# Kernel tuning notes

Measured on AMD Instinct MI355X. Metric: run time of the kernel, lower is better.

Reference implementation:

```python
import math
import jax, jax.numpy as jnp
from jax import lax
import numpy as np

B, HH, WW = 8, 128, 128
N = HH * WW
DIM, NH = 256, 4
HD = DIM // 2 // NH          # 32, per-head dim of the halved channels
CH = DIM // 2                # 128
THETA, MAXSEQ = 10000.0, 4096

# --- static FoPE frequency setup (mirrors RotaryEmbedding.get_inv_freq with fope=True) ---
def _inv_freq():
    rot = 2 * HD                                   # rotary dim = d_model//n_heads = 2*head_dim
    inv = 1.0 / THETA ** (np.arange(0, rot, 2, dtype=np.float64) / rot)
    return inv[inv >= 2.0 * np.pi / MAXSEQ].astype(np.float32)

INV_FREQ = _inv_freq()
D_IN = int(INV_FREQ.shape[0])                      # 23
D_OUT = D_IN if D_IN <= (2 * HD) // 4 else (2 * HD) // 4   # 16


def _coef(key, gain=0.5):
    # xavier_normal_ on (NH, D_IN, D_OUT) + step-eye offset, as in FourierEmbedding.__init__
    fan_in, fan_out = D_IN * D_OUT, NH * D_OUT
    std = gain * math.sqrt(2.0 / (fan_in + fan_out))
    c = std * jax.random.normal(key, (NH, D_IN, D_OUT), jnp.float32)
    step = math.ceil(D_IN / D_OUT)
    eye = np.zeros((NH, D_IN, D_OUT), np.float32)
    for i in range(D_OUT):
        if i * step < D_IN:
            eye[:, i * step, i] = 1.0
    return c + jnp.asarray(eye)


def setup_inputs() -> dict:
    key = jax.random.key(0)
    ks = jax.random.split(key, 10)
    def lin(k, o, i):
        lim = 1.0 / math.sqrt(i)
        return jax.random.uniform(k, (o, i), jnp.float32, -lim, lim)
    return {
        "x": jax.random.normal(ks[0], (B, N, DIM), jnp.float32),
        "Wq": lin(ks[1], CH, DIM), "bq": jnp.zeros((CH,), jnp.float32),
        "Wk": lin(ks[2], CH, DIM), "bk": jnp.zeros((CH,), jnp.float32),
        "Wv": lin(ks[3], CH, DIM), "bv": jnp.zeros((CH,), jnp.float32),
        # Hedgehog maps init as identity
        "Whq": jnp.eye(HD, dtype=jnp.float32), "bhq": jnp.zeros((HD,), jnp.float32),
        "Whk": jnp.eye(HD, dtype=jnp.float32), "bhk": jnp.zeros((HD,), jnp.float32),
        "sin_coef": _coef(ks[4]), "cos_coef": _coef(ks[5]),
        "lepe_w": 0.02 * jax.random.normal(ks[6], (CH, 1, 3, 3), jnp.float32),
        "lepe_b": jnp.zeros((CH,), jnp.float32),
        "temperature": jnp.ones((CH, 1), jnp.float32),
        "Wp": lin(ks[7], DIM, DIM), "bp": jnp.zeros((DIM,), jnp.float32),
        "h": HH, "w": WW,
    }


def _hedgehog(t, W, b):
    # t: [b,h,n,HD] -> [b,h,n,2*HD]
    y = jnp.einsum('bhnd,ed->bhne', t, W) + b
    return jax.nn.softmax(jnp.concatenate([2.0 * y, -2.0 * y], axis=-1), axis=-1)


def _fope(t, sin_coef, cos_coef, n):
    # t: [b,h,n,2*HD]; learnable Fourier rotary
    freqs = jnp.arange(n, dtype=jnp.float32)[:, None] * jnp.asarray(INV_FREQ)[None, :]  # [n,D_IN]
    cs = sin_coef / sin_coef.sum(axis=-2, keepdims=True)
    cc = cos_coef / cos_coef.sum(axis=-2, keepdims=True)
    fs = jnp.einsum('tD,hDd->htd', jnp.sin(freqs), cs)[None]   # [1,h,n,D_OUT]
    fc = jnp.einsum('tD,hDd->htd', jnp.cos(freqs), cc)[None]
    pad = ((0, 0), (0, 0), (0, 0), (0, HD - D_OUT))
    fs = jnp.pad(fs, pad, constant_values=1.0)
    fc = jnp.pad(fc, pad, constant_values=1.0)
    fs = jnp.concatenate([fs, fs], axis=-1)                    # [1,h,n,2*HD]
    fc = jnp.concatenate([fc, fc], axis=-1)
    x1, x2 = t[..., :HD], t[..., HD:]
    rot = jnp.concatenate([-x2, x1], axis=-1)
    return t * fc - rot * fs


def _forward(x, Wq, bq, Wk, bk, Wv, bv, Whq, bhq, Whk, bhk,
             sin_coef, cos_coef, lepe_w, lepe_b, temperature, Wp, bp, h, w):
    b, n, _ = x.shape
    q = x @ Wq.T + bq   # [b,n,CH]
    k = x @ Wk.T + bk
    v = x @ Wv.T + bv

    # ---- spatial brand (Hedgehog linear attention with Fourier rotary) ----
    qh = q.reshape(b, n, NH, HD).swapaxes(1, 2)   # [b,nh,n,HD]
    kh = k.reshape(b, n, NH, HD).swapaxes(1, 2)
    vh = v.reshape(b, n, NH, HD).swapaxes(1, 2)
    qf = _hedgehog(qh, Whq, bhq)                  # [b,nh,n,2HD]
    kf = _hedgehog(kh, Whk, bhk)
    q_fope = _fope(qf, sin_coef, cos_coef, n)
    k_fope = _fope(kf, sin_coef, cos_coef, n)
    kmean = kf.mean(axis=-2, keepdims=True)                       # [b,nh,1,2HD]
    z = 1.0 / (jnp.einsum('bhnd,bhsd->bhns', qf, kmean) + 1e-6)   # [b,nh,n,1]
    s = n ** (-0.5)
    kv = jnp.einsum('bhnd,bhne->bhde', k_fope * s, vh * s)        # [b,nh,2HD,HD]
    xs = jnp.einsum('bhnd,bhde->bhne', q_fope, kv) * z            # [b,nh,n,HD]
    xs = xs.swapaxes(1, 2).reshape(b, n, CH)
    v_img = vh.swapaxes(-1, -2).reshape(b, CH, h, w)
    conv = lax.conv_general_dilated(v_img, lepe_w, (1, 1), 'SAME',
                                    feature_group_count=CH,
                                    dimension_numbers=('NCHW', 'OIHW', 'NCHW'))
    conv = conv + lepe_b[None, :, None, None]
    x_spatial = conv.reshape(b, CH, n).transpose(0, 2, 1) + xs    # [b,n,CH]

    # ---- channel brand (transposed attention over channels) ----
    qc = q.swapaxes(-1, -2)   # [b,CH,n]
    kc = k.swapaxes(-1, -2)
    vc = v.swapaxes(-1, -2)
    qn = qc / jnp.maximum(jnp.linalg.norm(qc, axis=-1, keepdims=True), 1e-12)
    kn = kc / jnp.maximum(jnp.linalg.norm(kc, axis=-1, keepdims=True), 1e-12)
    attn = jax.nn.softmax(jnp.einsum('bcl,bdl->bcd', qn, kn) * temperature, axis=-1)
    x_channel = jnp.einsum('bcd,bdl->bcl', attn, vc).swapaxes(-1, -2)  # [b,n,CH]

    out = jnp.concatenate([x_spatial, x_channel], axis=-1) @ Wp.T + bp  # [b,n,DIM]
    return out, q, k


def reference(x, Wq, bq, Wk, bk, Wv, bv, Whq, bhq, Whk, bhk,
              sin_coef, cos_coef, lepe_w, lepe_b, temperature, Wp, bp, h, w):
    return _forward(x, Wq, bq, Wk, bk, Wv, bv, Whq, bhq, Whk, bhk,
                    sin_coef, cos_coef, lepe_w, lepe_b, temperature, Wp, bp, h, w)
```

## Files before the change

kernel.cpp:

```cpp
#include <hip/hip_runtime.h>
#include <cmath>

#define NB 8
#define NN 16384
#define DIN 23
#define DOUT 16

typedef short bf16x8 __attribute__((ext_vector_type(8)));
typedef float f32x4 __attribute__((ext_vector_type(4)));

__device__ __forceinline__ unsigned short f2bf(float f) {
    unsigned int u = __float_as_uint(f);
    u += 0x7FFFu + ((u >> 16) & 1u);
    return (unsigned short)(u >> 16);
}
__device__ __forceinline__ float bf2f(unsigned short s) {
    return __uint_as_float(((unsigned int)s) << 16);
}
__device__ __forceinline__ float rcpf(float x) { return __builtin_amdgcn_rcpf(x); }

__device__ __forceinline__ bf16x8 cvt8(float4 a, float4 b) {
    bf16x8 r;
    r[0]=(short)f2bf(a.x); r[1]=(short)f2bf(a.y); r[2]=(short)f2bf(a.z); r[3]=(short)f2bf(a.w);
    r[4]=(short)f2bf(b.x); r[5]=(short)f2bf(b.y); r[6]=(short)f2bf(b.z); r[7]=(short)f2bf(b.w);
    return r;
}
__device__ __forceinline__ void red16(f32x4& s) {
    #pragma unroll
    for (int off = 1; off < 16; off <<= 1) {
        s[0] += __shfl_xor(s[0], off); s[1] += __shfl_xor(s[1], off);
        s[2] += __shfl_xor(s[2], off); s[3] += __shfl_xor(s[3], off);
    }
}
__device__ __forceinline__ void red16x2(f32x4& s, f32x4& w) {
    #pragma unroll
    for (int off = 1; off < 16; off <<= 1) {
        s[0] += __shfl_xor(s[0], off); s[1] += __shfl_xor(s[1], off);
        s[2] += __shfl_xor(s[2], off); s[3] += __shfl_xor(s[3], off);
        w[0] += __shfl_xor(w[0], off); w[1] += __shfl_xor(w[1], off);
        w[2] += __shfl_xor(w[2], off); w[3] += __shfl_xor(w[3], off);
    }
}

#define WS_XSP    ((size_t)0)
#define WS_VB     ((size_t)16777216)
#define WS_XSB    ((size_t)25165824)
#define WS_FS     ((size_t)33554432)
#define WS_INV    ((size_t)35651584)
#define WS_CS     ((size_t)35651648)
#define WS_CC     ((size_t)35653184)
#define WS_WCAT   ((size_t)35654720)
#define WS_BCAT   ((size_t)35703872)
#define WS_KVPART ((size_t)35704256)
#define WS_KMPART ((size_t)37801408)
#define WS_KV     ((size_t)37866944)
#define WS_KMEAN  ((size_t)37932480)
#define WS_QN2    ((size_t)37934528)
#define WS_KN2    ((size_t)37935552)
#define WS_G      ((size_t)37936576)
#define WS_ATTN   ((size_t)38067648)
#define WS_BMATT  ((size_t)38198720)
#define WS_QB     ((size_t)38460864)
#define WS_KB     ((size_t)46849472)

__global__ void k_setup(const float* __restrict__ sc, const float* __restrict__ ccin,
                        float* __restrict__ inv, float* __restrict__ cs, float* __restrict__ cc)
{
    int t = threadIdx.x;
    if (t < DIN) inv[t] = (float)pow(10000.0, -((double)(2 * t)) / 64.0);
    int h = t >> 4, d = t & 15;
    float ss = 0.f, s2 = 0.f;
    for (int D = 0; D < DIN; ++D) { ss += sc[(h*DIN + D)*DOUT + d]; s2 += ccin[(h*DIN + D)*DOUT + d]; }
    float rs = 1.f / ss, r2 = 1.f / s2;
    for (int D = 0; D < DIN; ++D) {
        cs[(h*DIN + D)*DOUT + d] = sc[(h*DIN + D)*DOUT + d] * rs;
        cc[(h*DIN + D)*DOUT + d] = ccin[(h*DIN + D)*DOUT + d] * r2;
    }
}

__global__ __launch_bounds__(256) void k_tables(const float* __restrict__ inv, const float* __restrict__ cs,
                                                const float* __restrict__ cc,
                                                unsigned int* __restrict__ fsc)
{
    int t = threadIdx.x;
    int sub = t >> 6, lane = t & 63;
    int tpos = blockIdx.x*4 + sub;
    __shared__ float ssin[4][DIN], scos[4][DIN];
    if (lane < DIN) { float fr = (float)tpos * inv[lane]; ssin[sub][lane] = sinf(fr); scos[sub][lane] = cosf(fr); }
    __syncthreads();
    int h = lane >> 4, d = lane & 15;
    float as = 0.f, ac = 0.f;
    for (int D = 0; D < DIN; ++D) { as += ssin[sub][D]*cs[(h*DIN + D)*DOUT + d]; ac += scos[sub][D]*cc[(h*DIN + D)*DOUT + d]; }
    fsc[((size_t)h*NN + tpos)*16 + d] = ((unsigned int)f2bf(ac) << 16) | (unsigned int)f2bf(as);
}

__global__ __launch_bounds__(256) void k_wprep(
    const float* __restrict__ Wq, const float* __restrict__ Wk, const float* __restrict__ Wv,
    const float* __restrict__ bq, const float* __restrict__ bk, const float* __restrict__ bv,
    unsigned short* __restrict__ Wc, float* __restrict__ bcat)
{
    int row = blockIdx.x, t = threadIdx.x;
    const float* W = (row < 128) ? Wq : (row < 256) ? Wk : Wv;
    const float* bb = (row < 128) ? bq : (row < 256) ? bk : bv;
    int r = row & 127;
    Wc[(size_t)row*256 + t] = f2bf(W[(size_t)r*256 + t]);
    if (t == 0) bcat[row] = bb[r];
}

__global__ __launch_bounds__(256) void k_qkv_mfma(const float* __restrict__ x,
    const unsigned short* __restrict__ Wc, const float* __restrict__ bcat,
    float* __restrict__ q, float* __restrict__ k,
    unsigned short* __restrict__ qb, unsigned short* __restrict__ kb,
    unsigned short* __restrict__ vb)
{
    __shared__ unsigned short Asm[128*64];
    __shared__ unsigned short Bsm[128*64];
    int t = threadIdx.x;
    int lin = blockIdx.y*3 + blockIdx.x;
    int logical = (lin & 7)*384 + (lin >> 3);
    int ntile = logical % 3;
    int mtile = logical / 3;
    int m0 = mtile * 128;
    int n0 = ntile * 128;
    int wave = t >> 6, lane = t & 63;
    int wm = wave >> 1, wn = wave & 1;
    int lrow = lane & 15, lk = lane >> 4;
    f32x4 acc[4][4];
    #pragma unroll
    for (int i = 0; i < 4; ++i)
        #pragma unroll
        for (int j = 0; j < 4; ++j) acc[i][j] = (f32x4){0.f,0.f,0.f,0.f};

    int am = t >> 4, ak4 = t & 15;
    size_t arow = (size_t)(m0 + am);
    float4 pa[8];
    #pragma unroll
    for (int p = 0; p < 8; ++p)
        pa[p] = *reinterpret_cast<const float4*>(&x[(arow + p*16)*256 + ak4*4]);

    #pragma unroll
    for (int kt = 0; kt < 4; ++kt) {
        int k0 = kt * 64;
        if (kt) __syncthreads();
        #pragma unroll
        for (int p = 0; p < 8; ++p) {
            int m = am + p*16;
            ushort4 b4;
            b4.x = f2bf(pa[p].x); b4.y = f2bf(pa[p].y); b4.z = f2bf(pa[p].z); b4.w = f2bf(pa[p].w);
            int byte = m*128 + ((ak4*8) ^ ((m & 7) << 4));
            *reinterpret_cast<ushort4*>(reinterpret_cast<char*>(Asm) + byte) = b4;
        }
        {
            int n = t >> 3, k8 = t & 7;
            #pragma unroll
            for (int p = 0; p < 4; ++p, n += 32) {
                uint4 u4 = *reinterpret_cast<const uint4*>(&Wc[(size_t)(n0 + n)*256 + k0 + k8*8]);
                int byte = n*128 + ((k8 ^ (n & 7)) << 4);
                *reinterpret_cast<uint4*>(reinterpret_cast<char*>(Bsm) + byte) = u4;
            }
        }
        if (kt < 3) {
            #pragma unroll
            for (int p = 0; p < 8; ++p)
                pa[p] = *reinterpret_cast<const float4*>(&x[(arow + p*16)*256 + (kt+1)*64 + ak4*4]);
        }
        __syncthreads();
        #pragma unroll
        for (int ks = 0; ks < 2; ++ks) {
            bf16x8 af[4], bfv[4];
            #pragma unroll
            for (int mi = 0; mi < 4; ++mi) {
                int m = wm*64 + mi*16 + lrow;
                int u = (ks*4 + lk) ^ (m & 7);
                af[mi] = *reinterpret_cast<const bf16x8*>(reinterpret_cast<const char*>(Asm) + m*128 + u*16);
            }
            #pragma unroll
            for (int ni = 0; ni < 4; ++ni) {
                int n = wn*64 + ni*16 + lrow;
                int u = (ks*4 + lk) ^ (n & 7);
                bfv[ni] = *reinterpret_cast<const bf16x8*>(reinterpret_cast<const char*>(Bsm) + n*128 + u*16);
            }
            #pragma unroll
            for (int mi = 0; mi < 4; ++mi)
                #pragma unroll
                for (int ni = 0; ni < 4; ++ni)
                    acc[mi][ni] = __builtin_amdgcn_mfma_f32_16x16x32_bf16(af[mi], bfv[ni], acc[mi][ni], 0, 0, 0);
        }
    }
    #pragma unroll
    for (int mi = 0; mi < 4; ++mi) {
        #pragma unroll
        for (int ni = 0; ni < 4; ++ni) {
            int gcol = n0 + wn*64 + ni*16 + lrow;
            int c = gcol & 127;
            float bias = bcat[gcol];
            #pragma unroll
            for (int r = 0; r < 4; ++r) {
                size_t grow = (size_t)m0 + wm*64 + mi*16 + lk*4 + r;
                float val = acc[mi][ni][r] + bias;
                if (ntile == 0)      { q[grow*128 + c] = val; qb[grow*128 + c] = f2bf(val); }
                else if (ntile == 1) { k[grow*128 + c] = val; kb[grow*128 + c] = f2bf(val); }
                else                 vb[grow*128 + c] = f2bf(val);
            }
        }
    }
}

__global__ __launch_bounds__(256) void k_conv(const unsigned short* __restrict__ vb, const float* __restrict__ w,
                                              const float* __restrict__ bias, float* __restrict__ xsp)
{
    __shared__ float wsmT[9][128];
    __shared__ float bsm[128];
    int t = threadIdx.x;
    for (int i = t; i < 1152; i += 256) wsmT[i % 9][i / 9] = w[i];
    if (t < 128) bsm[t] = bias[t];
    __syncthreads();
    int jj = t >> 4, c8 = (t & 15) * 8;
    int j = blockIdx.x * 16 + jj;
    int i = blockIdx.y, b = blockIdx.z;
    float acc[8];
    #pragma unroll
    for (int l = 0; l < 8; ++l) acc[l] = bsm[c8 + l];
    #pragma unroll
    for (int di = 0; di < 3; ++di) {
        int ii = i + di - 1;
        if (ii < 0 || ii >= 128) continue;
        #pragma unroll
        for (int dj = 0; dj < 3; ++dj) {
            int jx = j + dj - 1;
            if (jx < 0 || jx >= 128) continue;
            uint4 u = *reinterpret_cast<const uint4*>(&vb[((size_t)b*NN + ii*128 + jx)*128 + c8]);
            const unsigned short* us = (const unsigned short*)&u;
            int kk = di*3 + dj;
            #pragma unroll
            for (int l = 0; l < 8; ++l)
                acc[l] += wsmT[kk][c8 + l] * bf2f(us[l]);
        }
    }
    float4 r0 = {acc[0],acc[1],acc[2],acc[3]}, r1 = {acc[4],acc[5],acc[6],acc[7]};
    size_t ob = ((size_t)b*NN + i*128 + j)*128 + c8;
    *reinterpret_cast<float4*>(&xsp[ob]) = r0;
    *reinterpret_cast<float4*>(&xsp[ob+4]) = r1;
}

__global__ __launch_bounds__(256) void k_featkv(
    const unsigned short* __restrict__ kb, const unsigned short* __restrict__ vb,
    const float* __restrict__ W, const float* __restrict__ bvec,
    const unsigned int* __restrict__ fsc,
    float* __restrict__ kvpart, float* __restrict__ kmpart)
{
    __shared__ __align__(16) unsigned short kfsT[4][64][72];
    __shared__ __align__(16) unsigned short vT[4][32][72];
    __shared__ float kms[4][64];
    int bh = blockIdx.y, b = bh >> 2, h = bh & 3;
    int chunk = blockIdx.x;
    int t = threadIdx.x, w = t >> 6, lane = t & 63;
    int c = lane & 15, g = lane >> 4;
    bf16x8 wb[2];
    #pragma unroll
    for (int et = 0; et < 2; ++et) {
        float4 wa = *reinterpret_cast<const float4*>(&W[(c + et*16)*32 + g*8]);
        float4 wb2 = *reinterpret_cast<const float4*>(&W[(c + et*16)*32 + g*8 + 4]);
        wb[et] = cvt8(wa, wb2);
    }
    float bias0 = bvec[c], bias1 = bvec[c + 16];
    f32x4 acc[4][2];
    #pragma unroll
    for (int i = 0; i < 4; ++i) { acc[i][0] = (f32x4){0.f,0.f,0.f,0.f}; acc[i][1] = (f32x4){0.f,0.f,0.f,0.f}; }
    f32x4 km0 = {0.f,0.f,0.f,0.f}, km1 = km0, km2 = km0, km3 = km0;

    for (int rnd = 0; rnd < 2; ++rnd) {
        int p0 = chunk*512 + w*128 + rnd*64;
        {
            uint4 vr[4];
            size_t vbase = ((size_t)(b*NN + p0 + c*4))*128 + h*32 + g*8;
            #pragma unroll
            for (int i = 0; i < 4; ++i) vr[i] = *reinterpret_cast<const uint4*>(&vb[vbase + (size_t)i*128]);
            #pragma unroll
            for (int j = 0; j < 8; ++j) {
                ushort4 pk;
                pk.x = ((const unsigned short*)&vr[0])[j];
                pk.y = ((const unsigned short*)&vr[1])[j];
                pk.z = ((const unsigned short*)&vr[2])[j];
                pk.w = ((const unsigned short*)&vr[3])[j];
                *reinterpret_cast<ushort4*>(&vT[w][g*8 + j][c*4]) = pk;
            }
        }
        #pragma unroll
        for (int mt = 0; mt < 4; ++mt) {
            int posA = p0 + mt*16 + c;
            bf16x8 af = *reinterpret_cast<const bf16x8*>(&kb[((size_t)(b*NN + posA))*128 + h*32 + g*8]);
            f32x4 z4 = {0.f,0.f,0.f,0.f};
            f32x4 y0 = __builtin_amdgcn_mfma_f32_16x16x32_bf16(af, wb[0], z4, 0, 0, 0);
            f32x4 y1 = __builtin_amdgcn_mfma_f32_16x16x32_bf16(af, wb[1], z4, 0, 0, 0);
            f32x4 el0, eh0, el1, eh1;
            #pragma unroll
            for (int r = 0; r < 4; ++r) {
                float a0 = 2.f*(y0[r] + bias0);
                float a1 = 2.f*(y1[r] + bias1);
                el0[r] = __expf(a0); eh0[r] = __expf(-a0);
                el1[r] = __expf(a1); eh1[r] = __expf(-a1);
            }
            f32x4 s = el0 + eh0 + el1 + eh1;
            red16(s);
            f32x4 rs;
            #pragma unroll
            for (int r = 0; r < 4; ++r) rs[r] = rcpf(s[r]);
            f32x4 klo0 = el0*rs, khi0 = eh0*rs, klo1 = el1*rs, khi1 = eh1*rs;
            km0 += klo0; km1 += khi0; km2 += klo1; km3 += khi1;
            int posC = p0 + mt*16 + g*4;
            ushort4 wlo0, whi0, wlo1, whi1;
            #pragma unroll
            for (int r = 0; r < 4; ++r) {
                unsigned int u = fsc[((size_t)h*NN + posC + r)*16 + c];
                float fsv = bf2f((unsigned short)(u & 0xffffu));
                float fcv = bf2f((unsigned short)(u >> 16));
                ((unsigned short*)&wlo0)[r] = f2bf(klo0[r]*fcv + khi0[r]*fsv);
                ((unsigned short*)&whi0)[r] = f2bf(khi0[r]*fcv - klo0[r]*fsv);
                ((unsigned short*)&wlo1)[r] = f2bf(klo1[r] + khi1[r]);
                ((unsigned short*)&whi1)[r] = f2bf(khi1[r] - klo1[r]);
            }
            int po = mt*16 + g*4;
            *reinterpret_cast<ushort4*>(&kfsT[w][c][po])      = wlo0;
            *reinterpret_cast<ushort4*>(&kfsT[w][32 + c][po]) = whi0;
            *reinterpret_cast<ushort4*>(&kfsT[w][16 + c][po]) = wlo1;
            *reinterpret_cast<ushort4*>(&kfsT[w][48 + c][po]) = whi1;
        }
        #pragma unroll
        for (int ks = 0; ks < 2; ++ks) {
            bf16x8 bf0 = *reinterpret_cast<const bf16x8*>(&vT[w][c][ks*32 + g*8]);
            bf16x8 bf1 = *reinterpret_cast<const bf16x8*>(&vT[w][16 + c][ks*32 + g*8]);
            #pragma unroll
            for (int mt = 0; mt < 4; ++mt) {
                bf16x8 af2 = *reinterpret_cast<const bf16x8*>(&kfsT[w][mt*16 + c][ks*32 + g*8]);
                acc[mt][0] = __builtin_amdgcn_mfma_f32_16x16x32_bf16(af2, bf0, acc[mt][0], 0, 0, 0);
                acc[mt][1] = __builtin_amdgcn_mfma_f32_16x16x32_bf16(af2, bf1, acc[mt][1], 0, 0, 0);
            }
        }
    }
    float kv0 = km0[0]+km0[1]+km0[2]+km0[3];
    float kv1 = km1[0]+km1[1]+km1[2]+km1[3];
    float kv2 = km2[0]+km2[1]+km2[2]+km2[3];
    float kv3 = km3[0]+km3[1]+km3[2]+km3[3];
    kv0 += __shfl_xor(kv0, 16); kv0 += __shfl_xor(kv0, 32);
    kv1 += __shfl_xor(kv1, 16); kv1 += __shfl_xor(kv1, 32);
    kv2 += __shfl_xor(kv2, 16); kv2 += __shfl_xor(kv2, 32);
    kv3 += __shfl_xor(kv3, 16); kv3 += __shfl_xor(kv3, 32);
    if (g == 0) {
        kms[w][c] = kv0; kms[w][16 + c] = kv2; kms[w][32 + c] = kv1; kms[w][48 + c] = kv3;
    }
    float* kvred = reinterpret_cast<float*>(&kfsT[0][0][0]);
    #pragma unroll
    for (int mt = 0; mt < 4; ++mt)
        #pragma unroll
        for (int nt = 0; nt < 2; ++nt) {
            int d = nt*16 + c;
            *reinterpret_cast<f32x4*>(&kvred[(size_t)(w*32 + d)*72 + mt*16 + g*4]) = acc[mt][nt];
        }
    __syncthreads();
    #pragma unroll
    for (int i = 0; i < 8; ++i) {
        int idx = t*8 + i;
        int f = idx >> 5, d = idx & 31;
        float s2 = kvred[(0*32 + d)*72 + f] + kvred[(1*32 + d)*72 + f]
                 + kvred[(2*32 + d)*72 + f] + kvred[(3*32 + d)*72 + f];
        kvpart[((size_t)(bh*32 + chunk))*2048 + idx] = s2;
    }
    if (t < 64) {
        float s2 = kms[0][t] + kms[1][t] + kms[2][t] + kms[3][t];
        kmpart[(size_t)(bh*32 + chunk)*64 + t] = s2;
    }
}

__global__ __launch_bounds__(256) void k_kvred2(const float* __restrict__ kvpart, unsigned short* __restrict__ kvT)
{
    int bh = blockIdx.x >> 3, part = blockIdx.x & 7;
    int idx = part*256 + threadIdx.x;
    float s = 0.f;
    for (int cidx = 0; cidx < 32; ++cidx) s += kvpart[((size_t)(bh*32 + cidx))*2048 + idx];
    int f = idx >> 5, d = idx & 31;
    kvT[(size_t)bh*2048 + d*64 + f] = f2bf(s * (1.f/16384.f));
}

__global__ __launch_bounds__(64) void k_kmred(const float* __restrict__ kmpart, float* __restrict__ kmean)
{
    int bh = blockIdx.x, t = threadIdx.x;
    float s = 0.f;
    for (int cidx = 0; cidx < 32; ++cidx) s += kmpart[(size_t)(bh*32 + cidx)*64 + t];
    kmean[bh*64 + t] = s * (1.f/16384.f);
}

__global__ __launch_bounds__(256) void k_featxs(
    const unsigned short* __restrict__ qb, const float* __restrict__ W, const float* __restrict__ bvec,
    const unsigned int* __restrict__ fsc, const unsigned short* __restrict__ kvT,
    const float* __restrict__ kmean, const float* __restrict__ xsp, unsigned short* __restrict__ xsb)
{
    __shared__ __align__(16) unsigned short qfs[4][64][72];
    int bh = blockIdx.y, b = bh >> 2, h = bh & 3;
    int chunk = blockIdx.x;
    int t = threadIdx.x, w = t >> 6, lane = t & 63;
    int c = lane & 15, g = lane >> 4;
    bf16x8 wb[2];
    #pragma unroll
    for (int et = 0; et < 2; ++et) {
        float4 wa = *reinterpret_cast<const float4*>(&W[(c + et*16)*32 + g*8]);
        float4 wb2 = *reinterpret_cast<const float4*>(&W[(c + et*16)*32 + g*8 + 4]);
        wb[et] = cvt8(wa, wb2);
    }
    float bias0 = bvec[c], bias1 = bvec[c + 16];
    float kml0 = kmean[bh*64 + c],      kml1 = kmean[bh*64 + 16 + c];
    float kmh0 = kmean[bh*64 + 32 + c], kmh1 = kmean[bh*64 + 48 + c];
    bf16x8 bkv[2][2];
    #pragma unroll
    for (int nt = 0; nt < 2; ++nt)
        #pragma unroll
        for (int ks = 0; ks < 2; ++ks)
            bkv[nt][ks] = *reinterpret_cast<const bf16x8*>(&kvT[(size_t)bh*2048 + (nt*16 + c)*64 + ks*32 + g*8]);

    for (int rnd = 0; rnd < 2; ++rnd) {
        int p0 = chunk*512 + w*128 + rnd*64;
        #pragma unroll
        for (int mt = 0; mt < 4; ++mt) {
            int posA = p0 + mt*16 + c;
            bf16x8 af = *reinterpret_cast<const bf16x8*>(&qb[((size_t)(b*NN + posA))*128 + h*32 + g*8]);
            f32x4 z4 = {0.f,0.f,0.f,0.f};
            f32x4 y0 = __builtin_amdgcn_mfma_f32_16x16x32_bf16(af, wb[0], z4, 0, 0, 0);
            f32x4 y1 = __builtin_amdgcn_mfma_f32_16x16x32_bf16(af, wb[1], z4, 0, 0, 0);
            f32x4 el0, eh0, el1, eh1;
            #pragma unroll
            for (int r = 0; r < 4; ++r) {
                float a0 = 2.f*(y0[r] + bias0);
                float a1 = 2.f*(y1[r] + bias1);
                el0[r] = __expf(a0); eh0[r] = __expf(-a0);
                el1[r] = __expf(a1); eh1[r] = __expf(-a1);
            }
            f32x4 s = el0 + eh0 + el1 + eh1;
            f32x4 wv = el0*kml0 + eh0*kmh0 + el1*kml1 + eh1*kmh1;
            red16x2(s, wv);
            f32x4 zr;
            #pragma unroll
            for (int r = 0; r < 4; ++r) {
                float rs = rcpf(s[r]);
                float z = rcpf(wv[r]*rs + 1e-6f);
                zr[r] = z*rs;
            }
            int posC = mt*16 + g*4;
            #pragma unroll
            for (int r = 0; r < 4; ++r) {
                unsigned int u = fsc[((size_t)h*NN + p0 + posC + r)*16 + c];
                float fsv = bf2f((unsigned short)(u & 0xffffu));
                float fcv = bf2f((unsigned short)(u >> 16));
                qfs[w][posC + r][c]      = f2bf(zr[r]*(el0[r]*fcv + eh0[r]*fsv));
                qfs[w][posC + r][32 + c] = f2bf(zr[r]*(eh0[r]*fcv - el0[r]*fsv));
                qfs[w][posC + r][16 + c] = f2bf(zr[r]*(el1[r] + eh1[r]));
                qfs[w][posC + r][48 + c] = f2bf(zr[r]*(eh1[r] - el1[r]));
            }
        }
        f32x4 acc[4][2];
        #pragma unroll
        for (int i = 0; i < 4; ++i) { acc[i][0] = (f32x4){0.f,0.f,0.f,0.f}; acc[i][1] = (f32x4){0.f,0.f,0.f,0.f}; }
        #pragma unroll
        for (int ks = 0; ks < 2; ++ks)
            #pragma unroll
            for (int mt = 0; mt < 4; ++mt) {
                bf16x8 af2 = *reinterpret_cast<const bf16x8*>(&qfs[w][mt*16 + c][ks*32 + g*8]);
                acc[mt][0] = __builtin_amdgcn_mfma_f32_16x16x32_bf16(af2, bkv[0][ks], acc[mt][0], 0, 0, 0);
                acc[mt][1] = __builtin_amdgcn_mfma_f32_16x16x32_bf16(af2, bkv[1][ks], acc[mt][1], 0, 0, 0);
            }
        #pragma unroll
        for (int mt = 0; mt < 4; ++mt)
            #pragma unroll
            for (int nt = 0; nt < 2; ++nt) {
                int d = nt*16 + c;
                #pragma unroll
                for (int r = 0; r < 4; ++r) {
                    int pos = p0 + mt*16 + g*4 + r;
                    size_t off = ((size_t)(b*NN + pos))*128 + h*32 + d;
                    xsb[off] = f2bf(xsp[off] + acc[mt][nt][r]);
                }
            }
    }
}

__global__ __launch_bounds__(256) void k_gram(const unsigned short* __restrict__ qb, const unsigned short* __restrict__ kb,
                                              float* __restrict__ Gpart,
                                              float* __restrict__ qn2, float* __restrict__ kn2)
{
    __shared__ unsigned short qTs[128][40];
    __shared__ unsigned short kTs[128][40];
    int kc = blockIdx.x, bb = blockIdx.y;
    int t = threadIdx.x, lane = t & 63;
    int wave = t >> 6, wm = wave >> 1, wn = wave & 1;
    int c = t & 127, lh = t >> 7;
    float qa = 0.f, ka = 0.f;
    f32x4 acc[4][4];
    #pragma unroll
    for (int i = 0; i < 4; ++i)
        #pragma unroll
        for (int j = 0; j < 4; ++j) acc[i][j] = (f32x4){0.f,0.f,0.f,0.f};

    for (int kt = 0; kt < 8; ++kt) {
        __syncthreads();
        #pragma unroll
        for (int i = 0; i < 16; ++i) {
            int l = lh*16 + i;
            size_t pos = (size_t)bb*NN + kc*256 + kt*32 + l;
            unsigned short qu = qb[pos*128 + c];
            unsigned short ku = kb[pos*128 + c];
            float qv = bf2f(qu), kvv = bf2f(ku);
            qa += qv*qv; ka += kvv*kvv;
            qTs[c][l] = qu;
            kTs[c][l] = ku;
        }
        __syncthreads();
        bf16x8 af[4];
        #pragma unroll
        for (int mi = 0; mi < 4; ++mi)
            af[mi] = *reinterpret_cast<const bf16x8*>(&qTs[wm*64 + mi*16 + (lane & 15)][(lane >> 4)*8]);
        #pragma unroll
        for (int ni = 0; ni < 4; ++ni) {
            bf16x8 bfr = *reinterpret_cast<const bf16x8*>(&kTs[wn*64 + ni*16 + (lane & 15)][(lane >> 4)*8]);
            #pragma unroll
            for (int mi = 0; mi < 4; ++mi)
                acc[mi][ni] = __builtin_amdgcn_mfma_f32_16x16x32_bf16(af[mi], bfr, acc[mi][ni], 0, 0, 0);
        }
    }
    size_t gb = ((size_t)(bb*64 + kc))*16384;
    #pragma unroll
    for (int mi = 0; mi < 4; ++mi) {
        #pragma unroll
        for (int ni = 0; ni < 4; ++ni) {
            int d = wn*64 + ni*16 + (lane & 15);
            #pragma unroll
            for (int r = 0; r < 4; ++r) {
                int cc = wm*64 + mi*16 + (lane >> 4)*4 + r;
                Gpart[gb + (size_t)cc*128 + d] = acc[mi][ni][r];
            }
        }
    }
    atomicAdd(&qn2[bb*128 + c], qa);
    atomicAdd(&kn2[bb*128 + c], ka);
}

__global__ __launch_bounds__(256) void k_gramred(const float* __restrict__ Gpart, float* __restrict__ G)
{
    int bb = blockIdx.y;
    int idx = blockIdx.x*256 + threadIdx.x;
    float s = 0.f;
    for (int kc = 0; kc < 64; ++kc) s += Gpart[((size_t)(bb*64 + kc))*16384 + idx];
    G[(size_t)bb*16384 + idx] = s;
}

__global__ __launch_bounds__(128) void k_attnsm(const float* __restrict__ G, const float* __restrict__ qn2,
    const float* __restrict__ kn2, const float* __restrict__ temp, float* __restrict__ attn)
{
    __shared__ float red[128];
    int row = blockIdx.x;
    int b = row >> 7, c = row & 127;
    int t = threadIdx.x;
    float qn = fmaxf(sqrtf(qn2[b*128 + c]), 1e-12f);
    float kn = fmaxf(sqrtf(kn2[b*128 + t]), 1e-12f);
    float val = G[(size_t)row*128 + t] / (qn*kn) * temp[c];
    red[t] = val; __syncthreads();
    for (int s = 64; s > 0; s >>= 1) { if (t < s) red[t] = fmaxf(red[t], red[t+s]); __syncthreads(); }
    float mm = red[0]; __syncthreads();
    float ev = expf(val - mm);
    red[t] = ev; __syncthreads();
    for (int s = 64; s > 0; s >>= 1) { if (t < s) red[t] += red[t+s]; __syncthreads(); }
    attn[(size_t)row*128 + t] = ev / red[0];
}

__global__ __launch_bounds__(256) void k_bmat(const float* __restrict__ attn, const float* __restrict__ Wp,
                                              unsigned short* __restrict__ BmatT)
{
    int b = blockIdx.y, kk = blockIdx.x, o = threadIdx.x;
    float val;
    if (kk < 128) {
        val = Wp[(size_t)o*256 + kk];
    } else {
        int d = kk - 128;
        __shared__ float a[128];
        if (o < 128) a[o] = attn[((size_t)b*128 + o)*128 + d];
        __syncthreads();
        float acc = 0.f;
        for (int c = 0; c < 128; ++c) acc += a[c] * Wp[(size_t)o*256 + 128 + c];
        val = acc;
    }
    BmatT[((size_t)b*256 + o)*256 + kk] = f2bf(val);
}

__global__ __launch_bounds__(256) void k_out_mfma(const unsigned short* __restrict__ xsb,
    const unsigned short* __restrict__ vb, const unsigned short* __restrict__ BmatT,
    const float* __restrict__ bp, float* __restrict__ out)
{
    __shared__ unsigned short Asm[128*64];
    __shared__ unsigned short Bsm[128*64];
    int t = threadIdx.x;
    int lin = blockIdx.y*2 + blockIdx.x;
    int logical = (lin & 7)*256 + (lin >> 3);
    int ntile = logical & 1;
    int mtile = logical >> 1;
    int m0 = mtile * 128;
    int n0 = ntile * 128;
    int b = mtile >> 7;
    int wave = t >> 6, lane = t & 63;
    int wm = wave >> 1, wn = wave & 1;
    int lrow = lane & 15, lk = lane >> 4;
    f32x4 acc[4][4];
    #pragma unroll
    for (int i = 0; i < 4; ++i)
        #pragma unroll
        for (int j = 0; j < 4; ++j) acc[i][j] = (f32x4){0.f,0.f,0.f,0.f};

    int am = t >> 3, ak8 = t & 7;
    uint4 pa4[4];
    #pragma unroll
    for (int p = 0; p < 4; ++p)
        pa4[p] = *reinterpret_cast<const uint4*>(&xsb[(size_t)(m0 + am + p*32)*128 + ak8*8]);

    #pragma unroll
    for (int kt = 0; kt < 4; ++kt) {
        if (kt) __syncthreads();
        #pragma unroll
        for (int p = 0; p < 4; ++p) {
            int m = am + p*32;
            int byte = m*128 + ((ak8 ^ (m & 7)) << 4);
            *reinterpret_cast<uint4*>(reinterpret_cast<char*>(Asm) + byte) = pa4[p];
        }
        {
            int n = t >> 3, k8 = t & 7;
            #pragma unroll
            for (int p = 0; p < 4; ++p, n += 32) {
                uint4 u4 = *reinterpret_cast<const uint4*>(&BmatT[((size_t)b*256 + n0 + n)*256 + kt*64 + k8*8]);
                int byte = n*128 + ((k8 ^ (n & 7)) << 4);
                *reinterpret_cast<uint4*>(reinterpret_cast<char*>(Bsm) + byte) = u4;
            }
        }
        if (kt < 3) {
            const unsigned short* Asrc = ((kt+1) < 2) ? xsb : vb;
            int ka0 = ((kt+1) & 1) * 64;
            #pragma unroll
            for (int p = 0; p < 4; ++p)
                pa4[p] = *reinterpret_cast<const uint4*>(&Asrc[(size_t)(m0 + am + p*32)*128 + ka0 + ak8*8]);
        }
        __syncthreads();
        #pragma unroll
        for (int ks = 0; ks < 2; ++ks) {
            bf16x8 af[4], bfv[4];
            #pragma unroll
            for (int mi = 0; mi < 4; ++mi) {
                int m = wm*64 + mi*16 + lrow;
                int u = (ks*4 + lk) ^ (m & 7);
                af[mi] = *reinterpret_cast<const bf16x8*>(reinterpret_cast<const char*>(Asm) + m*128 + u*16);
            }
            #pragma unroll
            for (int ni = 0; ni < 4; ++ni) {
                int n = wn*64 + ni*16 + lrow;
                int u = (ks*4 + lk) ^ (n & 7);
                bfv[ni] = *reinterpret_cast<const bf16x8*>(reinterpret_cast<const char*>(Bsm) + n*128 + u*16);
            }
            #pragma unroll
            for (int mi = 0; mi < 4; ++mi)
                #pragma unroll
                for (int ni = 0; ni < 4; ++ni)
                    acc[mi][ni] = __builtin_amdgcn_mfma_f32_16x16x32_bf16(af[mi], bfv[ni], acc[mi][ni], 0, 0, 0);
        }
    }
    #pragma unroll
    for (int mi = 0; mi < 4; ++mi) {
        #pragma unroll
        for (int ni = 0; ni < 4; ++ni) {
            int gcol = n0 + wn*64 + ni*16 + lrow;
            float bias = bp[gcol];
            #pragma unroll
            for (int r = 0; r < 4; ++r) {
                size_t grow = (size_t)m0 + wm*64 + mi*16 + lk*4 + r;
                out[grow*256 + gcol] = acc[mi][ni][r] + bias;
            }
        }
    }
}

extern "C" void kernel_launch(void* const* d_in, const int* in_sizes, int n_in,
                              void* d_out, int out_size, void* d_ws, size_t ws_size,
                              hipStream_t stream)
{
    (void)in_sizes; (void)n_in; (void)out_size; (void)ws_size;
    const float* x    = (const float*)d_in[0];
    const float* Wq   = (const float*)d_in[1];
    const float* bq   = (const float*)d_in[2];
    const float* Wk   = (const float*)d_in[3];
    const float* bk   = (const float*)d_in[4];
    const float* Wv   = (const float*)d_in[5];
    const float* bv   = (const float*)d_in[6];
    const float* Whq  = (const float*)d_in[7];
    const float* bhq  = (const float*)d_in[8];
    const float* Whk  = (const float*)d_in[9];
    const float* bhk  = (const float*)d_in[10];
    const float* sinc = (const float*)d_in[11];
    const float* cosc = (const float*)d_in[12];
    const float* lw   = (const float*)d_in[13];
    const float* lb   = (const float*)d_in[14];
    const float* temp = (const float*)d_in[15];
    const float* Wp   = (const float*)d_in[16];
    const float* bp   = (const float*)d_in[17];

    float* out = (float*)d_out;
    float* q   = out + 33554432;
    float* k   = out + 50331648;
    float* ws  = (float*)d_ws;

    float* xsp    = ws + WS_XSP;
    float* Gpart  = ws + WS_XSP;
    unsigned short* vbuf = (unsigned short*)(ws + WS_VB);
    unsigned short* xsb  = (unsigned short*)(ws + WS_XSB);
    unsigned int* fsc = (unsigned int*)(ws + WS_FS);
    float* inv    = ws + WS_INV;
    float* cs     = ws + WS_CS;
    float* cc     = ws + WS_CC;
    unsigned short* Wc = (unsigned short*)(ws + WS_WCAT);
    float* bcat   = ws + WS_BCAT;
    float* kvpart = ws + WS_KVPART;
    float* kmpart = ws + WS_KMPART;
    unsigned short* kvT = (unsigned short*)(ws + WS_KV);
    float* kmean  = ws + WS_KMEAN;
    float* qn2    = ws + WS_QN2;
    float* kn2    = ws + WS_KN2;
    float* G      = ws + WS_G;
    float* attn   = ws + WS_ATTN;
    unsigned short* BmatT = (unsigned short*)(ws + WS_BMATT);
    unsigned short* qbuf  = (unsigned short*)(ws + WS_QB);
    unsigned short* kbuf  = (unsigned short*)(ws + WS_KB);

    hipMemsetAsync(qn2, 0, 2048*sizeof(float), stream);

    k_setup<<<1, 64, 0, stream>>>(sinc, cosc, inv, cs, cc);
    k_tables<<<4096, 256, 0, stream>>>(inv, cs, cc, fsc);
    k_wprep<<<384, 256, 0, stream>>>(Wq, Wk, Wv, bq, bk, bv, Wc, bcat);
    k_qkv_mfma<<<dim3(3, 1024), 256, 0, stream>>>(x, Wc, bcat, q, k, qbuf, kbuf, vbuf);
    k_conv<<<dim3(8, 128, 8), 256, 0, stream>>>(vbuf, lw, lb, xsp);
    k_featkv<<<dim3(32, 32), 256, 0, stream>>>(kbuf, vbuf, Whk, bhk, fsc, kvpart, kmpart);
    k_kvred2<<<256, 256, 0, stream>>>(kvpart, kvT);
    k_kmred<<<32, 64, 0, stream>>>(kmpart, kmean);
    k_featxs<<<dim3(32, 32), 256, 0, stream>>>(qbuf, Whq, bhq, fsc, kvT, kmean, xsp, xsb);
    k_gram<<<dim3(64, 8), 256, 0, stream>>>(qbuf, kbuf, Gpart, qn2, kn2);
    k_gramred<<<dim3(64, 8), 256, 0, stream>>>(Gpart, G);
    k_attnsm<<<1024, 128, 0, stream>>>(G, qn2, kn2, temp, attn);
    k_bmat<<<dim3(256, 8), 256, 0, stream>>>(attn, Wp, BmatT);
    k_out_mfma<<<dim3(2, 1024), 256, 0, stream>>>(xsb, vbuf, BmatT, bp, out);
}
```

Baseline: 440.2 us.

## Store conv output as bf16, shrink feature tiles, fold reduction kernels

The depthwise conv output is now stored in bf16 instead of fp32, halving its write and later read traffic in the feature kernel. The featkv and featxs kernels process 32-position rounds instead of 64, which shrinks the shared-memory tiles and may raise occupancy. The kmean reduction is folded into kvred2 and the Gram partial reduction into the softmax kernel, removing two launches and the intermediate G buffer. The bf16 storage of the conv output adds rounding error before the residual add.

New measurement: 384.8 us, median of 4. 1.14x faster.

```diff
diff --git a/kernel.cpp b/kernel.cpp
--- a/kernel.cpp
+++ b/kernel.cpp
@@ -42,7 +42,8 @@
     }
 }
 
-#define WS_XSP    ((size_t)0)
+#define WS_XSPB   ((size_t)0)
+#define WS_GPART  ((size_t)8388608)
 #define WS_VB     ((size_t)16777216)
 #define WS_XSB    ((size_t)25165824)
 #define WS_FS     ((size_t)33554432)
@@ -57,7 +58,6 @@
 #define WS_KMEAN  ((size_t)37932480)
 #define WS_QN2    ((size_t)37934528)
 #define WS_KN2    ((size_t)37935552)
-#define WS_G      ((size_t)37936576)
 #define WS_ATTN   ((size_t)38067648)
 #define WS_BMATT  ((size_t)38198720)
 #define WS_QB     ((size_t)38460864)
@@ -207,7 +207,7 @@
 }
 
 __global__ __launch_bounds__(256) void k_conv(const unsigned short* __restrict__ vb, const float* __restrict__ w,
-                                              const float* __restrict__ bias, float* __restrict__ xsp)
+                                              const float* __restrict__ bias, unsigned short* __restrict__ xspb)
 {
     __shared__ float wsmT[9][128];
     __shared__ float bsm[128];
@@ -237,10 +237,12 @@
                 acc[l] += wsmT[kk][c8 + l] * bf2f(us[l]);
         }
     }
-    float4 r0 = {acc[0],acc[1],acc[2],acc[3]}, r1 = {acc[4],acc[5],acc[6],acc[7]};
+    ushort4 r0, r1;
+    r0.x = f2bf(acc[0]); r0.y = f2bf(acc[1]); r0.z = f2bf(acc[2]); r0.w = f2bf(acc[3]);
+    r1.x = f2bf(acc[4]); r1.y = f2bf(acc[5]); r1.z = f2bf(acc[6]); r1.w = f2bf(acc[7]);
     size_t ob = ((size_t)b*NN + i*128 + j)*128 + c8;
-    *reinterpret_cast<float4*>(&xsp[ob]) = r0;
-    *reinterpret_cast<float4*>(&xsp[ob+4]) = r1;
+    *reinterpret_cast<ushort4*>(&xspb[ob]) = r0;
+    *reinterpret_cast<ushort4*>(&xspb[ob+4]) = r1;
 }
 
 __global__ __launch_bounds__(256) void k_featkv(
@@ -249,13 +251,14 @@
     const unsigned int* __restrict__ fsc,
     float* __restrict__ kvpart, float* __restrict__ kmpart)
 {
-    __shared__ __align__(16) unsigned short kfsT[4][64][72];
-    __shared__ __align__(16) unsigned short vT[4][32][72];
+    __shared__ __align__(16) char smem[34816];
     __shared__ float kms[4][64];
     int bh = blockIdx.y, b = bh >> 2, h = bh & 3;
     int chunk = blockIdx.x;
     int t = threadIdx.x, w = t >> 6, lane = t & 63;
     int c = lane & 15, g = lane >> 4;
+    unsigned short* kfsTw = reinterpret_cast<unsigned short*>(smem) + w*2560;
+    unsigned short* vTw   = reinterpret_cast<unsigned short*>(smem + 20480) + w*1280;
     bf16x8 wb[2];
     #pragma unroll
     for (int et = 0; et < 2; ++et) {
@@ -269,25 +272,23 @@
     for (int i = 0; i < 4; ++i) { acc[i][0] = (f32x4){0.f,0.f,0.f,0.f}; acc[i][1] = (f32x4){0.f,0.f,0.f,0.f}; }
     f32x4 km0 = {0.f,0.f,0.f,0.f}, km1 = km0, km2 = km0, km3 = km0;
 
-    for (int rnd = 0; rnd < 2; ++rnd) {
-        int p0 = chunk*512 + w*128 + rnd*64;
+    for (int rnd = 0; rnd < 4; ++rnd) {
+        int p0 = chunk*512 + w*128 + rnd*32;
         {
-            uint4 vr[4];
-            size_t vbase = ((size_t)(b*NN + p0 + c*4))*128 + h*32 + g*8;
-            #pragma unroll
-            for (int i = 0; i < 4; ++i) vr[i] = *reinterpret_cast<const uint4*>(&vb[vbase + (size_t)i*128]);
+            uint4 vr0, vr1;
+            size_t vbase = ((size_t)(b*NN + p0 + c*2))*128 + h*32 + g*8;
+            vr0 = *reinterpret_cast<const uint4*>(&vb[vbase]);
+            vr1 = *reinterpret_cast<const uint4*>(&vb[vbase + 128]);
             #pragma unroll
             for (int j = 0; j < 8; ++j) {
-                ushort4 pk;
-                pk.x = ((const unsigned short*)&vr[0])[j];
-                pk.y = ((const unsigned short*)&vr[1])[j];
-                pk.z = ((const unsigned short*)&vr[2])[j];
-                pk.w = ((const unsigned short*)&vr[3])[j];
-                *reinterpret_cast<ushort4*>(&vT[w][g*8 + j][c*4]) = pk;
-            }
-        }
-        #pragma unroll
-        for (int mt = 0; mt < 4; ++mt) {
+                ushort2 pk;
+                pk.x = ((const unsigned short*)&vr0)[j];
+                pk.y = ((const unsigned short*)&vr1)[j];
+                *reinterpret_cast<ushort2*>(&vTw[(g*8 + j)*40 + c*2]) = pk;
+            }
+        }
+        #pragma unroll
+        for (int mt = 0; mt < 2; ++mt) {
             int posA = p0 + mt*16 + c;
             bf16x8 af = *reinterpret_cast<const bf16x8*>(&kb[((size_t)(b*NN + posA))*128 + h*32 + g*8]);
             f32x4 z4 = {0.f,0.f,0.f,0.f};
@@ -321,18 +322,17 @@
                 ((unsigned short*)&whi1)[r] = f2bf(khi1[r] - klo1[r]);
             }
             int po = mt*16 + g*4;
-            *reinterpret_cast<ushort4*>(&kfsT[w][c][po])      = wlo0;
-            *reinterpret_cast<ushort4*>(&kfsT[w][32 + c][po]) = whi0;
-            *reinterpret_cast<ushort4*>(&kfsT[w][16 + c][po]) = wlo1;
-            *reinterpret_cast<ushort4*>(&kfsT[w][48 + c][po]) = whi1;
-        }
-        #pragma unroll
-        for (int ks = 0; ks < 2; ++ks) {
-            bf16x8 bf0 = *reinterpret_cast<const bf16x8*>(&vT[w][c][ks*32 + g*8]);
-            bf16x8 bf1 = *reinterpret_cast<const bf16x8*>(&vT[w][16 + c][ks*32 + g*8]);
+            *reinterpret_cast<ushort4*>(&kfsTw[(c)*40 + po])      = wlo0;
+            *reinterpret_cast<ushort4*>(&kfsTw[(32 + c)*40 + po]) = whi0;
+            *reinterpret_cast<ushort4*>(&kfsTw[(16 + c)*40 + po]) = wlo1;
+            *reinterpret_cast<ushort4*>(&kfsTw[(48 + c)*40 + po]) = whi1;
+        }
+        {
+            bf16x8 bf0 = *reinterpret_cast<const bf16x8*>(&vTw[(c)*40 + g*8]);
+            bf16x8 bf1 = *reinterpret_cast<const bf16x8*>(&vTw[(16 + c)*40 + g*8]);
             #pragma unroll
             for (int mt = 0; mt < 4; ++mt) {
-                bf16x8 af2 = *reinterpret_cast<const bf16x8*>(&kfsT[w][mt*16 + c][ks*32 + g*8]);
+                bf16x8 af2 = *reinterpret_cast<const bf16x8*>(&kfsTw[(mt*16 + c)*40 + g*8]);
                 acc[mt][0] = __builtin_amdgcn_mfma_f32_16x16x32_bf16(af2, bf0, acc[mt][0], 0, 0, 0);
                 acc[mt][1] = __builtin_amdgcn_mfma_f32_16x16x32_bf16(af2, bf1, acc[mt][1], 0, 0, 0);
             }
@@ -349,21 +349,22 @@
     if (g == 0) {
         kms[w][c] = kv0; kms[w][16 + c] = kv2; kms[w][32 + c] = kv1; kms[w][48 + c] = kv3;
     }
-    float* kvred = reinterpret_cast<float*>(&kfsT[0][0][0]);
+    __syncthreads();
+    float* kvred = reinterpret_cast<float*>(smem);
     #pragma unroll
     for (int mt = 0; mt < 4; ++mt)
         #pragma unroll
         for (int nt = 0; nt < 2; ++nt) {
             int d = nt*16 + c;
-            *reinterpret_cast<f32x4*>(&kvred[(size_t)(w*32 + d)*72 + mt*16 + g*4]) = acc[mt][nt];
+            *reinterpret_cast<f32x4*>(&kvred[(size_t)(w*32 + d)*68 + mt*16 + g*4]) = acc[mt][nt];
         }
     __syncthreads();
     #pragma unroll
     for (int i = 0; i < 8; ++i) {
         int idx = t*8 + i;
         int f = idx >> 5, d = idx & 31;
-        float s2 = kvred[(0*32 + d)*72 + f] + kvred[(1*32 + d)*72 + f]
-                 + kvred[(2*32 + d)*72 + f] + kvred[(3*32 + d)*72 + f];
+        float s2 = kvred[(0*32 + d)*68 + f] + kvred[(1*32 + d)*68 + f]
+                 + kvred[(2*32 + d)*68 + f] + kvred[(3*32 + d)*68 + f];
         kvpart[((size_t)(bh*32 + chunk))*2048 + idx] = s2;
     }
     if (t < 64) {
@@ -372,7 +373,8 @@
     }
 }
 
-__global__ __launch_bounds__(256) void k_kvred2(const float* __restrict__ kvpart, unsigned short* __restrict__ kvT)
+__global__ __launch_bounds__(256) void k_kvred2(const float* __restrict__ kvpart, const float* __restrict__ kmpart,
+                                                unsigned short* __restrict__ kvT, float* __restrict__ kmean)
 {
     int bh = blockIdx.x >> 3, part = blockIdx.x & 7;
     int idx = part*256 + threadIdx.x;
@@ -380,22 +382,20 @@
     for (int cidx = 0; cidx < 32; ++cidx) s += kvpart[((size_t)(bh*32 + cidx))*2048 + idx];
     int f = idx >> 5, d = idx & 31;
     kvT[(size_t)bh*2048 + d*64 + f] = f2bf(s * (1.f/16384.f));
-}
-
-__global__ __launch_bounds__(64) void k_kmred(const float* __restrict__ kmpart, float* __restrict__ kmean)
-{
-    int bh = blockIdx.x, t = threadIdx.x;
-    float s = 0.f;
-    for (int cidx = 0; cidx < 32; ++cidx) s += kmpart[(size_t)(bh*32 + cidx)*64 + t];
-    kmean[bh*64 + t] = s * (1.f/16384.f);
+    if (part == 0 && threadIdx.x < 64) {
+        int tt = threadIdx.x;
+        float sm = 0.f;
+        for (int cidx = 0; cidx < 32; ++cidx) sm += kmpart[(size_t)(bh*32 + cidx)*64 + tt];
+        kmean[bh*64 + tt] = sm * (1.f/16384.f);
+    }
 }
 
 __global__ __launch_bounds__(256) void k_featxs(
     const unsigned short* __restrict__ qb, const float* __restrict__ W, const float* __restrict__ bvec,
     const unsigned int* __restrict__ fsc, const unsigned short* __restrict__ kvT,
-    const float* __restrict__ kmean, const float* __restrict__ xsp, unsigned short* __restrict__ xsb)
-{
-    __shared__ __align__(16) unsigned short qfs[4][64][72];
+    const float* __restrict__ kmean, const unsigned short* __restrict__ xspb, unsigned short* __restrict__ xsb)
+{
+    __shared__ __align__(16) unsigned short qfs[4][32][72];
     int bh = blockIdx.y, b = bh >> 2, h = bh & 3;
     int chunk = blockIdx.x;
     int t = threadIdx.x, w = t >> 6, lane = t & 63;
@@ -417,10 +417,10 @@
         for (int ks = 0; ks < 2; ++ks)
             bkv[nt][ks] = *reinterpret_cast<const bf16x8*>(&kvT[(size_t)bh*2048 + (nt*16 + c)*64 + ks*32 + g*8]);
 
-    for (int rnd = 0; rnd < 2; ++rnd) {
-        int p0 = chunk*512 + w*128 + rnd*64;
-        #pragma unroll
-        for (int mt = 0; mt < 4; ++mt) {
+    for (int rnd = 0; rnd < 4; ++rnd) {
+        int p0 = chunk*512 + w*128 + rnd*32;
+        #pragma unroll
+        for (int mt = 0; mt < 2; ++mt) {
             int posA = p0 + mt*16 + c;
             bf16x8 af = *reinterpret_cast<const bf16x8*>(&qb[((size_t)(b*NN + posA))*128 + h*32 + g*8]);
             f32x4 z4 = {0.f,0.f,0.f,0.f};
@@ -456,19 +456,19 @@
                 qfs[w][posC + r][48 + c] = f2bf(zr[r]*(eh1[r] - el1[r]));
             }
         }
-        f32x4 acc[4][2];
-        #pragma unroll
-        for (int i = 0; i < 4; ++i) { acc[i][0] = (f32x4){0.f,0.f,0.f,0.f}; acc[i][1] = (f32x4){0.f,0.f,0.f,0.f}; }
+        f32x4 acc[2][2];
+        #pragma unroll
+        for (int i = 0; i < 2; ++i) { acc[i][0] = (f32x4){0.f,0.f,0.f,0.f}; acc[i][1] = (f32x4){0.f,0.f,0.f,0.f}; }
         #pragma unroll
         for (int ks = 0; ks < 2; ++ks)
             #pragma unroll
-            for (int mt = 0; mt < 4; ++mt) {
+            for (int mt = 0; mt < 2; ++mt) {
                 bf16x8 af2 = *reinterpret_cast<const bf16x8*>(&qfs[w][mt*16 + c][ks*32 + g*8]);
                 acc[mt][0] = __builtin_amdgcn_mfma_f32_16x16x32_bf16(af2, bkv[0][ks], acc[mt][0], 0, 0, 0);
                 acc[mt][1] = __builtin_amdgcn_mfma_f32_16x16x32_bf16(af2, bkv[1][ks], acc[mt][1], 0, 0, 0);
             }
         #pragma unroll
-        for (int mt = 0; mt < 4; ++mt)
+        for (int mt = 0; mt < 2; ++mt)
             #pragma unroll
             for (int nt = 0; nt < 2; ++nt) {
                 int d = nt*16 + c;
@@ -476,7 +476,7 @@
                 for (int r = 0; r < 4; ++r) {
                     int pos = p0 + mt*16 + g*4 + r;
                     size_t off = ((size_t)(b*NN + pos))*128 + h*32 + d;
-                    xsb[off] = f2bf(xsp[off] + acc[mt][nt][r]);
+                    xsb[off] = f2bf(bf2f(xspb[off]) + acc[mt][nt][r]);
                 }
             }
     }
@@ -542,25 +542,19 @@
     atomicAdd(&kn2[bb*128 + c], ka);
 }
 
-__global__ __launch_bounds__(256) void k_gramred(const float* __restrict__ Gpart, float* __restrict__ G)
-{
-    int bb = blockIdx.y;
-    int idx = blockIdx.x*256 + threadIdx.x;
-    float s = 0.f;
-    for (int kc = 0; kc < 64; ++kc) s += Gpart[((size_t)(bb*64 + kc))*16384 + idx];
-    G[(size_t)bb*16384 + idx] = s;
-}
-
-__global__ __launch_bounds__(128) void k_attnsm(const float* __restrict__ G, const float* __restrict__ qn2,
+__global__ __launch_bounds__(128) void k_attnsm(const float* __restrict__ Gpart, const float* __restrict__ qn2,
     const float* __restrict__ kn2, const float* __restrict__ temp, float* __restrict__ attn)
 {
     __shared__ float red[128];
     int row = blockIdx.x;
     int b = row >> 7, c = row & 127;
     int t = threadIdx.x;
+    float s0 = 0.f;
+    for (int kc = 0; kc < 64; ++kc)
+        s0 += Gpart[((size_t)(b*64 + kc))*16384 + (size_t)c*128 + t];
     float qn = fmaxf(sqrtf(qn2[b*128 + c]), 1e-12f);
     float kn = fmaxf(sqrtf(kn2[b*128 + t]), 1e-12f);
-    float val = G[(size_t)row*128 + t] / (qn*kn) * temp[c];
+    float val = s0 / (qn*kn) * temp[c];
     red[t] = val; __syncthreads();
     for (int s = 64; s > 0; s >>= 1) { if (t < s) red[t] = fmaxf(red[t], red[t+s]); __syncthreads(); }
     float mm = red[0]; __syncthreads();
@@ -710,8 +704,8 @@
     float* k   = out + 50331648;
     float* ws  = (float*)d_ws;
 
-    float* xsp    = ws + WS_XSP;
-    float* Gpart  = ws + WS_XSP;
+    unsigned short* xspb = (unsigned short*)(ws + WS_XSPB);
+    float* Gpart  = ws + WS_GPART;
     unsigned short* vbuf = (unsigned short*)(ws + WS_VB);
     unsigned short* xsb  = (unsigned short*)(ws + WS_XSB);
     unsigned int* fsc = (unsigned int*)(ws + WS_FS);
@@ -726,7 +720,6 @@
     float* kmean  = ws + WS_KMEAN;
     float* qn2    = ws + WS_QN2;
     float* kn2    = ws + WS_KN2;
-    float* G      = ws + WS_G;
     float* attn   = ws + WS_ATTN;
     unsigned short* BmatT = (unsigned short*)(ws + WS_BMATT);
     unsigned short* qbuf  = (unsigned short*)(ws + WS_QB);
@@ -738,14 +731,12 @@
     k_tables<<<4096, 256, 0, stream>>>(inv, cs, cc, fsc);
     k_wprep<<<384, 256, 0, stream>>>(Wq, Wk, Wv, bq, bk, bv, Wc, bcat);
     k_qkv_mfma<<<dim3(3, 1024), 256, 0, stream>>>(x, Wc, bcat, q, k, qbuf, kbuf, vbuf);
-    k_conv<<<dim3(8, 128, 8), 256, 0, stream>>>(vbuf, lw, lb, xsp);
+    k_conv<<<dim3(8, 128, 8), 256, 0, stream>>>(vbuf, lw, lb, xspb);
     k_featkv<<<dim3(32, 32), 256, 0, stream>>>(kbuf, vbuf, Whk, bhk, fsc, kvpart, kmpart);
-    k_kvred2<<<256, 256, 0, stream>>>(kvpart, kvT);
-    k_kmred<<<32, 64, 0, stream>>>(kmpart, kmean);
-    k_featxs<<<dim3(32, 32), 256, 0, stream>>>(qbuf, Whq, bhq, fsc, kvT, kmean, xsp, xsb);
+    k_kvred2<<<256, 256, 0, stream>>>(kvpart, kmpart, kvT, kmean);
+    k_featxs<<<dim3(32, 32), 256, 0, stream>>>(qbuf, Whq, bhq, fsc, kvT, kmean, xspb, xsb);
     k_gram<<<dim3(64, 8), 256, 0, stream>>>(qbuf, kbuf, Gpart, qn2, kn2);
-    k_gramred<<<dim3(64, 8), 256, 0, stream>>>(Gpart, G);
-    k_attnsm<<<1024, 128, 0, stream>>>(G, qn2, kn2, temp, attn);
+    k_attnsm<<<1024, 128, 0, stream>>>(Gpart, qn2, kn2, temp, attn);
     k_bmat<<<dim3(256, 8), 256, 0, stream>>>(attn, Wp, BmatT);
     k_out_mfma<<<dim3(2, 1024), 256, 0, stream>>>(xsb, vbuf, BmatT, bp, out);
 }
```
